# Kernel tuning notes

Measured on AMD Instinct MI355X. Metric: run time of the kernel, lower is better.

## Reference

```python
import jax, jax.numpy as jnp
import numpy as np

B, S, CC, CF, E, H, NH = 16, 1024, 8, 8, 64, 1024, 16
DH = H // NH
VOCAB = 10000
EPS = 1e-5


def layer_norm(x, g, b):
    m = x.mean(-1, keepdims=True)
    v = x.var(-1, keepdims=True)
    return (x - m) / jnp.sqrt(v + EPS) * g + b


def setup_inputs():
    key = jax.random.key(0)
    ks = jax.random.split(key, 30)
    f32 = jnp.float32
    n = lambda k, shp, s=0.02: jax.random.normal(k, shp, f32) * s
    inp = {}
    inp['cate_x'] = jax.random.randint(ks[0], (B, S, CC), 0, VOCAB)
    inp['cont_x'] = jax.random.normal(ks[1], (B, S, CF), f32)
    inp['mask'] = jax.random.randint(ks[2], (B, S), 0, 2)
    # parameters
    inp['emb_table'] = n(ks[3], (VOCAB, E)).at[0].set(0.0)  # padding_idx=0
    inp['cate_W'] = n(ks[4], (CC * E, H)); inp['cate_b'] = jnp.zeros((H,), f32)
    inp['cate_ln_g'] = jnp.ones((H,), f32); inp['cate_ln_b'] = jnp.zeros((H,), f32)
    inp['bn_g'] = jnp.ones((CF,), f32); inp['bn_b'] = jnp.zeros((CF,), f32)
    inp['cont_W'] = n(ks[5], (CF, H)); inp['cont_b'] = jnp.zeros((H,), f32)
    inp['cont_ln_g'] = jnp.ones((H,), f32); inp['cont_ln_b'] = jnp.zeros((H,), f32)
    inp['comb_W'] = n(ks[6], (2 * H, H)); inp['comb_b'] = jnp.zeros((H,), f32)
    inp['comb_ln_g'] = jnp.ones((H,), f32); inp['comb_ln_b'] = jnp.zeros((H,), f32)
    inp['Wq'] = n(ks[7], (H, H)); inp['bq'] = jnp.zeros((H,), f32)
    inp['Wk'] = n(ks[8], (H, H)); inp['bk'] = jnp.zeros((H,), f32)
    inp['Wv'] = n(ks[9], (H, H)); inp['bv'] = jnp.zeros((H,), f32)
    inp['Wo'] = n(ks[10], (H, H)); inp['bo'] = jnp.zeros((H,), f32)
    return inp


def reference(cate_x, cont_x, mask, emb_table, cate_W, cate_b, cate_ln_g, cate_ln_b,
              bn_g, bn_b, cont_W, cont_b, cont_ln_g, cont_ln_b,
              comb_W, comb_b, comb_ln_g, comb_ln_b,
              Wq, bq, Wk, bk, Wv, bv, Wo, bo):
    # categorical path: embed -> flatten cols -> Linear+LN
    cate_emb = emb_table[cate_x].reshape(B, S, CC * E)
    cate_h = layer_norm(cate_emb @ cate_W + cate_b, cate_ln_g, cate_ln_b)
    # continuous path: BatchNorm1d over flattened (B*S, CF) with batch stats
    xf = cont_x.reshape(-1, CF)
    mu = xf.mean(0)
    var = xf.var(0)  # biased, as torch BN normalization
    xn = ((xf - mu) / jnp.sqrt(var + EPS) * bn_g + bn_b).reshape(B, S, CF)
    cont_h = layer_norm(xn @ cont_W + cont_b, cont_ln_g, cont_ln_b)
    # combine: ReLU -> Linear -> LN
    seq = jax.nn.relu(jnp.concatenate([cate_h, cont_h], axis=2))
    x = layer_norm(seq @ comb_W + comb_b, comb_ln_g, comb_ln_b)  # [B,S,H]
    # multi-head attention (dropout is identity in eval)
    Q = (x @ Wq + bq).reshape(B, S, NH, DH)
    K = (x @ Wk + bk).reshape(B, S, NH, DH)
    V = (x @ Wv + bv).reshape(B, S, NH, DH)
    scores = jnp.einsum('bqhd,bkhd->bhqk', Q, K) / np.sqrt(DH).astype(np.float32)
    # faithful to source: mask broadcast over the QUERY axis
    scores = jnp.where(mask[:, None, :, None] == 0, -1e7, scores)
    attn = jax.nn.softmax(scores, axis=-1)
    out = jnp.einsum('bhqk,bkhd->bqhd', attn, V).reshape(B, S, H)
    out = out @ Wo + bo
    return out[:, -1:, -1]  # [B,1]
```

## Files before the change

### kernel.cpp

```cpp
#include <hip/hip_runtime.h>
#include <hip/hip_bf16.h>
#include <math.h>

#define EPS 1e-5f

typedef unsigned short u16;
typedef __attribute__((ext_vector_type(8))) short bf16x8;
typedef __attribute__((ext_vector_type(4))) float f32x4;

__device__ __forceinline__ float b2f(u16 u) {
  union { unsigned int i; float f; } v; v.i = ((unsigned int)u) << 16; return v.f;
}
__device__ __forceinline__ u16 f2b(float f) {
  union { float f; unsigned int i; } v; v.f = f;
  unsigned int r = v.i + 0x7fff + ((v.i >> 16) & 1);
  return (u16)(r >> 16);
}

__device__ __forceinline__ void gload_lds16(const u16* g, u16* l) {
  __builtin_amdgcn_global_load_lds(
      (const __attribute__((address_space(1))) unsigned int*)g,
      (__attribute__((address_space(3))) unsigned int*)l, 16, 0, 0);
}

__global__ __launch_bounds__(256) void prep_k(
    const float* __restrict__ cx, float* __restrict__ part_bn,
    float* __restrict__ outacc, float* __restrict__ Sall,
    const float* __restrict__ emb, u16* __restrict__ embb,
    const float* __restrict__ cate_W, u16* __restrict__ cateWT) {
  __shared__ float shmem[64 * 65];
  const int bid = blockIdx.x, tid = threadIdx.x;

  if (bid == 0) {
    if (tid < 16) outacc[tid] = 0.f;
    for (int i = tid; i < 544; i += 256) Sall[i] = 0.f;
    return;
  }
  if (bid <= 64) {
    int pb = bid - 1;
    int gid = pb * 256 + tid;
    float4 a = ((const float4*)cx)[2 * gid];
    float4 b = ((const float4*)cx)[2 * gid + 1];
    float v[16];
    v[0] = a.x; v[1] = a.y; v[2] = a.z; v[3] = a.w;
    v[4] = b.x; v[5] = b.y; v[6] = b.z; v[7] = b.w;
#pragma unroll
    for (int i = 0; i < 8; ++i) v[8 + i] = v[i] * v[i];
#pragma unroll
    for (int off = 32; off; off >>= 1)
#pragma unroll
      for (int i = 0; i < 16; ++i) v[i] += __shfl_down(v[i], off);
    int l = tid & 63, wv_ = tid >> 6;
    if (l == 0)
#pragma unroll
      for (int i = 0; i < 16; ++i) shmem[wv_ * 16 + i] = v[i];
    __syncthreads();
    if (tid < 16)
      part_bn[pb * 16 + tid] = shmem[tid] + shmem[16 + tid] + shmem[32 + tid] + shmem[48 + tid];
    return;
  }
  if (bid <= 689) {
    int i = (bid - 65) * 256 + tid;
    if (i < 160000) {
      float4 v = ((const float4*)emb)[i];
      ushort4 u; u.x = f2b(v.x); u.y = f2b(v.y); u.z = f2b(v.z); u.w = f2b(v.w);
      ((ushort4*)embb)[i] = u;
    }
    return;
  }
  {
    int local = bid - 690;
    int n0 = (local & 15) * 64, k0 = (local >> 4) * 64;
    int c = tid & 63, r0 = tid >> 6;
#pragma unroll
    for (int i = 0; i < 16; ++i) {
      int r = r0 + i * 4;
      shmem[r * 65 + c] = cate_W[(size_t)(k0 + r) * 1024 + n0 + c];
    }
    __syncthreads();
#pragma unroll
    for (int i = 0; i < 16; ++i) {
      int r = r0 + i * 4;
      cateWT[(size_t)(n0 + r) * 512 + k0 + c] = f2b(shmem[c * 65 + r]);
    }
  }
}

template <int MODE>
__global__ __launch_bounds__(512) void gemm256(
    const u16* __restrict__ A0, const u16* __restrict__ A1,
    const int* __restrict__ idx, const u16* __restrict__ embb,
    const u16* __restrict__ BT, const float* __restrict__ bias,
    u16* __restrict__ C, int K) {
  __shared__ u16 As[2][2][8192];
  __shared__ u16 Bs[2][2][8192];
  __shared__ int sidx[MODE == 1 ? 2048 : 4];
  const int tid = threadIdx.x;
  const int bid = blockIdx.x;
  const int chunk = gridDim.x >> 3;
  const int swz = (bid & 7) * chunk + (bid >> 3);
  const int row0 = (swz >> 2) * 256;
  const int col0 = (swz & 3) * 256;

  const int rr8 = tid >> 3;
  const int p8  = tid & 7;
  const int sl  = p8 ^ (rr8 & 7);

  const int l   = tid & 63;
  const int w   = tid >> 6;
  const int wrh = w >> 2;
  const int wcq = w & 3;
  const int hb  = wcq >> 1;
  const int rbb = (wcq & 1) * 64;
  const int lr  = l & 15;
  const int lk  = l >> 4;

  f32x4 acc[8][4];
#pragma unroll
  for (int m = 0; m < 8; ++m)
#pragma unroll
    for (int n = 0; n < 4; ++n) acc[m][n] = (f32x4){0.f, 0.f, 0.f, 0.f};

  const int nt = K >> 6;
  const int nit = nt >> 1;

  if (MODE == 1) {
    *(int4*)&sidx[tid * 4] = *(const int4*)&idx[row0 * 8 + tid * 4];
    __syncthreads();
  }

  auto stageA = [&](int t, int h) {
    const int k0 = t << 6;
    const int buf = t & 1;
#pragma unroll
    for (int i = 0; i < 2; ++i) {
      const u16* asrc;
      if (MODE == 1) {
        int id = sidx[(h * 128 + i * 64 + rr8) * 8 + (k0 >> 6)];
        asrc = embb + (size_t)id * 64 + sl * 8;
      } else {
        int ar = row0 + h * 128 + i * 64 + rr8;
        const u16* base = (k0 < 1024) ? A0 : A1;
        asrc = base + (size_t)ar * 1024 + (k0 & 1023) + sl * 8;
      }
      gload_lds16(asrc, &As[buf][h][i * 4096 + tid * 8]);
    }
  };
  auto stageB = [&](int t, int h) {
    const int k0 = t << 6;
    const int buf = t & 1;
#pragma unroll
    for (int i = 0; i < 2; ++i) {
      int br = col0 + h * 128 + i * 64 + rr8;
      gload_lds16(BT + (size_t)br * K + k0 + sl * 8,
                  &Bs[buf][h][i * 4096 + tid * 8]);
    }
  };

  bf16x8 bfr[4][2];
  auto loadB = [&](int buf) {
#pragma unroll
    for (int n = 0; n < 4; ++n)
#pragma unroll
      for (int ks = 0; ks < 2; ++ks) {
        int rowb = rbb + n * 16 + lr;
        int ph = (ks * 4 + lk) ^ (lr & 7);
        bfr[n][ks] = *(const bf16x8*)&Bs[buf][hb][rowb * 64 + ph * 8];
      }
  };
  auto loadA = [&](bf16x8 (&af)[2][2], int buf, int q) {
#pragma unroll
    for (int mm = 0; mm < 2; ++mm)
#pragma unroll
      for (int ks = 0; ks < 2; ++ks) {
        int rowa = (q * 2 + mm) * 16 + lr;
        int ph = (ks * 4 + lk) ^ (lr & 7);
        af[mm][ks] = *(const bf16x8*)&As[buf][wrh][rowa * 64 + ph * 8];
      }
  };
  auto mfma_quad = [&](bf16x8 (&af)[2][2], int q) {
    __builtin_amdgcn_s_setprio(1);
#pragma unroll
    for (int ks = 0; ks < 2; ++ks)
#pragma unroll
      for (int mm = 0; mm < 2; ++mm)
#pragma unroll
        for (int n = 0; n < 4; ++n)
          acc[q * 2 + mm][n] = __builtin_amdgcn_mfma_f32_16x16x32_bf16(
              af[mm][ks], bfr[n][ks], acc[q * 2 + mm][n], 0, 0, 0);
    __builtin_amdgcn_s_setprio(0);
  };

  stageA(0, 0); stageA(0, 1);
  stageB(0, 0); stageB(0, 1);
  stageB(1, 0); stageB(1, 1);
  asm volatile("s_waitcnt vmcnt(4)" ::: "memory");
  __builtin_amdgcn_s_barrier();

  for (int it = 0; it < nit; ++it) {
    const int T = it * 2;
    const bool more = (T + 2 < nt);
    bf16x8 af[2][2];

    loadB(0); loadA(af, 0, 0);
    stageA(T + 1, 0);
    __builtin_amdgcn_s_barrier();
    asm volatile("s_waitcnt lgkmcnt(0)" ::: "memory");
    mfma_quad(af, 0);
    __builtin_amdgcn_s_barrier();
    loadA(af, 0, 1);
    stageA(T + 1, 1);
    __builtin_amdgcn_s_barrier();
    asm volatile("s_waitcnt lgkmcnt(0)" ::: "memory");
    mfma_quad(af, 1);
    __builtin_amdgcn_s_barrier();
    loadA(af, 0, 2);
    if (more) stageB(T + 2, 0);
    __builtin_amdgcn_s_barrier();
    asm volatile("s_waitcnt lgkmcnt(0)" ::: "memory");
    mfma_quad(af, 2);
    __builtin_amdgcn_s_barrier();
    loadA(af, 0, 3);
    if (more) stageB(T + 2, 1);
    __builtin_amdgcn_s_barrier();
    asm volatile("s_waitcnt lgkmcnt(0)" ::: "memory");
    mfma_quad(af, 3);
    if (more) asm volatile("s_waitcnt vmcnt(4)" ::: "memory");
    else      asm volatile("s_waitcnt vmcnt(0)" ::: "memory");
    __builtin_amdgcn_s_barrier();

    loadB(1); loadA(af, 1, 0);
    if (more) stageA(T + 2, 0);
    __builtin_amdgcn_s_barrier();
    asm volatile("s_waitcnt lgkmcnt(0)" ::: "memory");
    mfma_quad(af, 0);
    __builtin_amdgcn_s_barrier();
    loadA(af, 1, 1);
    if (more) stageA(T + 2, 1);
    __builtin_amdgcn_s_barrier();
    asm volatile("s_waitcnt lgkmcnt(0)" ::: "memory");
    mfma_quad(af, 1);
    __builtin_amdgcn_s_barrier();
    loadA(af, 1, 2);
    if (more) stageB(T + 3, 0);
    __builtin_amdgcn_s_barrier();
    asm volatile("s_waitcnt lgkmcnt(0)" ::: "memory");
    mfma_quad(af, 2);
    __builtin_amdgcn_s_barrier();
    loadA(af, 1, 3);
    if (more) stageB(T + 3, 1);
    __builtin_amdgcn_s_barrier();
    asm volatile("s_waitcnt lgkmcnt(0)" ::: "memory");
    mfma_quad(af, 3);
    if (it + 1 < nit) {
      asm volatile("s_waitcnt vmcnt(4)" ::: "memory");
      __builtin_amdgcn_s_barrier();
    }
  }

  float bv_[4];
#pragma unroll
  for (int n = 0; n < 4; ++n) bv_[n] = bias[col0 + wcq * 64 + n * 16 + lr];
#pragma unroll
  for (int m = 0; m < 8; ++m) {
#pragma unroll
    for (int n = 0; n < 4; ++n) {
      int cc = col0 + wcq * 64 + n * 16 + lr;
#pragma unroll
      for (int q4 = 0; q4 < 4; ++q4) {
        int rr = row0 + wrh * 128 + m * 16 + lk * 4 + q4;
        C[(size_t)rr * 1024 + cc] = f2b(acc[m][n][q4] + bv_[n]);
      }
    }
  }
}

__global__ __launch_bounds__(256) void stat_k(const u16* __restrict__ buf,
                                              float* __restrict__ stats) {
  int tid = threadIdx.x;
  int lane = tid & 63, wave = tid >> 6;
  size_t row = (size_t)blockIdx.x * 4 + wave;
  const u16* p = buf + row * 1024 + lane * 16;
  uint4 u0 = *(const uint4*)p;
  uint4 u1 = *(const uint4*)(p + 8);
  float s = 0.f, s2 = 0.f;
#pragma unroll
  for (int i = 0; i < 4; ++i) {
    unsigned int w0 = ((unsigned int*)&u0)[i];
    unsigned int w1 = ((unsigned int*)&u1)[i];
    float a0 = b2f((u16)(w0 & 0xffff)), a1 = b2f((u16)(w0 >> 16));
    float a2 = b2f((u16)(w1 & 0xffff)), a3 = b2f((u16)(w1 >> 16));
    s += a0 + a1 + a2 + a3;
    s2 += a0 * a0 + a1 * a1 + a2 * a2 + a3 * a3;
  }
#pragma unroll
  for (int off = 32; off; off >>= 1) { s += __shfl_xor(s, off); s2 += __shfl_xor(s2, off); }
  if (lane == 0) {
    float mean = s * (1.f / 1024.f);
    float var = s2 * (1.f / 1024.f) - mean * mean;
    stats[row * 2] = mean;
    stats[row * 2 + 1] = rsqrtf(var + EPS);
  }
}

__device__ __forceinline__ void ln_body(u16* __restrict__ buf,
                                        const float* __restrict__ g,
                                        const float* __restrict__ b, int relu,
                                        int blk, int tid) {
  int lane = tid & 63, wave = tid >> 6;
  size_t row = (size_t)blk * 4 + wave;
  u16* p = buf + row * 1024 + lane * 16;
  uint4 u0 = *(uint4*)p;
  uint4 u1 = *(uint4*)(p + 8);
  float x[16];
#pragma unroll
  for (int i = 0; i < 4; ++i) {
    unsigned int w0 = ((unsigned int*)&u0)[i];
    unsigned int w1 = ((unsigned int*)&u1)[i];
    x[2 * i]     = b2f((u16)(w0 & 0xffff));
    x[2 * i + 1] = b2f((u16)(w0 >> 16));
    x[8 + 2 * i]     = b2f((u16)(w1 & 0xffff));
    x[8 + 2 * i + 1] = b2f((u16)(w1 >> 16));
  }
  float s = 0.f, s2 = 0.f;
#pragma unroll
  for (int i = 0; i < 16; ++i) { s += x[i]; s2 += x[i] * x[i]; }
#pragma unroll
  for (int off = 32; off; off >>= 1) { s += __shfl_xor(s, off); s2 += __shfl_xor(s2, off); }
  float mean = s * (1.f / 1024.f);
  float var = s2 * (1.f / 1024.f) - mean * mean;
  float rs = rsqrtf(var + EPS);
  float y[16];
#pragma unroll
  for (int q = 0; q < 4; ++q) {
    float4 gv = *(const float4*)(g + lane * 16 + q * 4);
    float4 bv = *(const float4*)(b + lane * 16 + q * 4);
    y[4 * q]     = (x[4 * q]     - mean) * rs * gv.x + bv.x;
    y[4 * q + 1] = (x[4 * q + 1] - mean) * rs * gv.y + bv.y;
    y[4 * q + 2] = (x[4 * q + 2] - mean) * rs * gv.z + bv.z;
    y[4 * q + 3] = (x[4 * q + 3] - mean) * rs * gv.w + bv.w;
  }
  if (relu)
#pragma unroll
    for (int i = 0; i < 16; ++i) y[i] = fmaxf(y[i], 0.f);
  uint4 o0, o1;
#pragma unroll
  for (int i = 0; i < 4; ++i) {
    ((unsigned int*)&o0)[i] = (unsigned int)f2b(y[2 * i]) | ((unsigned int)f2b(y[2 * i + 1]) << 16);
    ((unsigned int*)&o1)[i] = (unsigned int)f2b(y[8 + 2 * i]) | ((unsigned int)f2b(y[8 + 2 * i + 1]) << 16);
  }
  *(uint4*)p = o0;
  *(uint4*)(p + 8) = o1;
}

__device__ __forceinline__ void cont_body(const float* __restrict__ cx,
                                          const float* __restrict__ part_bn,
                                          const float* __restrict__ bn_g,
                                          const float* __restrict__ bn_b,
                                          const float* __restrict__ W,
                                          const float* __restrict__ cb,
                                          const float* __restrict__ g,
                                          const float* __restrict__ bb,
                                          u16* __restrict__ out,
                                          int row0, int tid) {
  __shared__ float sp[4][16];
  __shared__ float tt[16];
  __shared__ float ab[2][8];
  __shared__ float xn[8][8];
  __shared__ float rr1[4][8], rr2[4][8];

  if (tid < 64) {
    int f = tid & 15, qd = tid >> 4;
    float s = 0.f;
    for (int j = qd * 16; j < qd * 16 + 16; ++j) s += part_bn[j * 16 + f];
    sp[qd][f] = s;
  }
  __syncthreads();
  if (tid < 16) tt[tid] = sp[0][tid] + sp[1][tid] + sp[2][tid] + sp[3][tid];
  __syncthreads();
  if (tid < 8) {
    float mu = tt[tid] * (1.f / 16384.f);
    float var = tt[8 + tid] * (1.f / 16384.f) - mu * mu;
    float a = rsqrtf(var + EPS) * bn_g[tid];
    ab[0][tid] = a;
    ab[1][tid] = bn_b[tid] - mu * a;
  }
  __syncthreads();
  if (tid < 64) {
    int r = tid >> 3, f = tid & 7;
    xn[r][f] = ab[0][f] * cx[(row0 + r) * 8 + f] + ab[1][f];
  }
  __syncthreads();

  int c = tid * 4;
  float4 cbv = *(const float4*)(cb + c);
  float acc[8][4];
#pragma unroll
  for (int r = 0; r < 8; ++r) {
    acc[r][0] = cbv.x; acc[r][1] = cbv.y; acc[r][2] = cbv.z; acc[r][3] = cbv.w;
  }
  for (int k = 0; k < 8; ++k) {
    float4 w4 = *(const float4*)(W + k * 1024 + c);
#pragma unroll
    for (int r = 0; r < 8; ++r) {
      float xv = xn[r][k];
      acc[r][0] = fmaf(xv, w4.x, acc[r][0]);
      acc[r][1] = fmaf(xv, w4.y, acc[r][1]);
      acc[r][2] = fmaf(xv, w4.z, acc[r][2]);
      acc[r][3] = fmaf(xv, w4.w, acc[r][3]);
    }
  }
  float s1[8], s2[8];
#pragma unroll
  for (int r = 0; r < 8; ++r) {
    s1[r] = acc[r][0] + acc[r][1] + acc[r][2] + acc[r][3];
    s2[r] = acc[r][0] * acc[r][0] + acc[r][1] * acc[r][1] +
            acc[r][2] * acc[r][2] + acc[r][3] * acc[r][3];
  }
#pragma unroll
  for (int off = 32; off; off >>= 1)
#pragma unroll
    for (int r = 0; r < 8; ++r) {
      s1[r] += __shfl_down(s1[r], off);
      s2[r] += __shfl_down(s2[r], off);
    }
  int lane = tid & 63, wv = tid >> 6;
  if (lane == 0)
#pragma unroll
    for (int r = 0; r < 8; ++r) { rr1[wv][r] = s1[r]; rr2[wv][r] = s2[r]; }
  __syncthreads();
  float4 gv = *(const float4*)(g + c);
  float4 bv = *(const float4*)(bb + c);
#pragma unroll
  for (int r = 0; r < 8; ++r) {
    float ss = rr1[0][r] + rr1[1][r] + rr1[2][r] + rr1[3][r];
    float qq = rr2[0][r] + rr2[1][r] + rr2[2][r] + rr2[3][r];
    float mean = ss * (1.f / 1024.f);
    float var = qq * (1.f / 1024.f) - mean * mean;
    float rs = rsqrtf(var + EPS);
    float y0 = fmaxf((acc[r][0] - mean) * rs * gv.x + bv.x, 0.f);
    float y1 = fmaxf((acc[r][1] - mean) * rs * gv.y + bv.y, 0.f);
    float y2 = fmaxf((acc[r][2] - mean) * rs * gv.z + bv.z, 0.f);
    float y3 = fmaxf((acc[r][3] - mean) * rs * gv.w + bv.w, 0.f);
    ushort4 o; o.x = f2b(y0); o.y = f2b(y1); o.z = f2b(y2); o.w = f2b(y3);
    *(ushort4*)(out + (size_t)(row0 + r) * 1024 + c) = o;
  }
}

__global__ __launch_bounds__(256) void mid_k(
    u16* __restrict__ X1, const float* __restrict__ cate_g,
    const float* __restrict__ cate_bb,
    const float* __restrict__ comb_W, u16* __restrict__ combWT,
    const float* __restrict__ Wv, const float* __restrict__ Wo,
    const float* __restrict__ comb_g, const float* __restrict__ comb_bbv,
    u16* __restrict__ wvob_hi, u16* __restrict__ wvob_lo,
    float* __restrict__ woc, float* __restrict__ Swg, float* __restrict__ Swb,
    const float* __restrict__ cx, const float* __restrict__ part_bn,
    const float* __restrict__ bn_g, const float* __restrict__ bn_b,
    const float* __restrict__ cont_W, const float* __restrict__ cont_b,
    const float* __restrict__ cont_g, const float* __restrict__ cont_bb,
    u16* __restrict__ X2) {
  __shared__ float shmem[64 * 65];
  const int bid = blockIdx.x, tid = threadIdx.x;
  if (bid < 4096) {
    ln_body(X1, cate_g, cate_bb, 1, bid, tid);
    return;
  }
  if (bid < 4608) {
    int local = bid - 4096;
    int n0 = (local & 15) * 64, k0 = (local >> 4) * 64;
    int c = tid & 63, r0 = tid >> 6;
#pragma unroll
    for (int i = 0; i < 16; ++i) {
      int r = r0 + i * 4;
      shmem[r * 65 + c] = comb_W[(size_t)(k0 + r) * 1024 + n0 + c];
    }
    __syncthreads();
#pragma unroll
    for (int i = 0; i < 16; ++i) {
      int r = r0 + i * 4;
      combWT[(size_t)(n0 + r) * 2048 + k0 + c] = f2b(shmem[c * 65 + r]);
    }
    return;
  }
  if (bid < 4672) {
    int local = bid - 4608;
    int h = local >> 2, jc = local & 3;
    if (tid < 64) shmem[tid] = Wo[(size_t)(h * 64 + tid) * 1024 + 1023];
    __syncthreads();
    if (jc == 0 && tid < 64) woc[h * 64 + tid] = shmem[tid];
    int j = jc * 256 + tid;
    const float* vr = Wv + (size_t)j * 1024 + h * 64;
    float s = 0.f;
    for (int d4 = 0; d4 < 64; d4 += 4) {
      float4 w4 = *(const float4*)(vr + d4);
      s = fmaf(w4.x, shmem[d4], s);
      s = fmaf(w4.y, shmem[d4 + 1], s);
      s = fmaf(w4.z, shmem[d4 + 2], s);
      s = fmaf(w4.w, shmem[d4 + 3], s);
    }
    float sg_ = s * comb_g[j];
    u16 hi = f2b(sg_);
    float lo = sg_ - b2f(hi);
    wvob_hi[h * 1024 + j] = hi;
    wvob_lo[h * 1024 + j] = f2b(lo);
    float swgp = sg_;
    float swbp = s * comb_bbv[j];
#pragma unroll
    for (int off = 32; off; off >>= 1) {
      swgp += __shfl_down(swgp, off);
      swbp += __shfl_down(swbp, off);
    }
    int lane = tid & 63, wv = tid >> 6;
    if (lane == 0) { shmem[64 + wv] = swgp; shmem[68 + wv] = swbp; }
    __syncthreads();
    if (tid == 0) {
      atomicAdd(&Swg[h], shmem[64] + shmem[65] + shmem[66] + shmem[67]);
      atomicAdd(&Swb[h], shmem[68] + shmem[69] + shmem[70] + shmem[71]);
    }
    return;
  }
  {
    int row0 = (bid - 4672) * 8;
    cont_body(cx, part_bn, bn_g, bn_b, cont_W, cont_b, cont_g, cont_bb, X2,
              row0, tid);
  }
}

__global__ __launch_bounds__(256) void qproj_k(const u16* __restrict__ x,
                                               const float* __restrict__ stats,
                                               const float* __restrict__ g,
                                               const float* __restrict__ bb,
                                               const float* __restrict__ Wq,
                                               const float* __restrict__ bq,
                                               float* __restrict__ q) {
  __shared__ u16 xs[16][1024];
  __shared__ float part[16][16][16];
  __shared__ float sm[16], sr[16];
  int tid = threadIdx.x;
  if (tid < 16) {
    size_t row = (size_t)tid * 1024 + 1023;
    sm[tid] = stats[row * 2];
    sr[tid] = stats[row * 2 + 1];
  }
  __syncthreads();
  for (int i = tid; i < 4096; i += 256) {
    int b = i >> 8, off = (i & 255) * 4;
    ushort4 u =
        *(const ushort4*)(x + ((size_t)(b * 1024 + 1023)) * 1024 + off);
    float4 gv = *(const float4*)(g + off);
    float4 bv = *(const float4*)(bb + off);
    float m = sm[b], r = sr[b];
    ushort4 o;
    o.x = f2b((b2f(u.x) - m) * r * gv.x + bv.x);
    o.y = f2b((b2f(u.y) - m) * r * gv.y + bv.y);
    o.z = f2b((b2f(u.z) - m) * r * gv.z + bv.z);
    o.w = f2b((b2f(u.w) - m) * r * gv.w + bv.w);
    *(ushort4*)&xs[b][off] = o;
  }
  __syncthreads();
  int c = tid & 15;
  int col = blockIdx.x * 16 + c;
  int kq = tid >> 4;
  float acc[16];
#pragma unroll
  for (int b = 0; b < 16; ++b) acc[b] = 0.f;
  for (int k = kq * 64; k < kq * 64 + 64; ++k) {
    float wv = Wq[(size_t)k * 1024 + col];
#pragma unroll
    for (int b = 0; b < 16; ++b) acc[b] = fmaf(b2f(xs[b][k]), wv, acc[b]);
  }
#pragma unroll
  for (int b = 0; b < 16; ++b) part[kq][b][c] = acc[b];
  __syncthreads();
  {
    int b = tid >> 4, cc = tid & 15;
    float s = 0.f;
#pragma unroll
    for (int j = 0; j < 16; ++j) s += part[j][b][cc];
    q[b * 1024 + blockIdx.x * 16 + cc] = s + bq[blockIdx.x * 16 + cc];
  }
}

__global__ __launch_bounds__(256) void kq_k(const float* __restrict__ Wk,
                                            const float* __restrict__ bk,
                                            const float* __restrict__ q,
                                            const float* __restrict__ g,
                                            const float* __restrict__ bb,
                                            u16* __restrict__ qtb,
                                            float* __restrict__ bkq,
                                            float* __restrict__ Sg,
                                            float* __restrict__ Sb) {
  int h = blockIdx.x >> 2, jc = blockIdx.x & 3;
  int tid = threadIdx.x;
  __shared__ float Qs[16][64];
  __shared__ float rg[4][16], rb[4][16];
  for (int i = tid; i < 1024; i += 256) {
    int b = i >> 6, d = i & 63;
    Qs[b][d] = q[b * 1024 + h * 64 + d];
  }
  __syncthreads();
  int j = jc * 256 + tid;
  float acc[16];
#pragma unroll
  for (int b = 0; b < 16; ++b) acc[b] = 0.f;
  const float* wr = Wk + (size_t)j * 1024 + h * 64;
  for (int d4 = 0; d4 < 64; d4 += 4) {
    float4 w4 = *(const float4*)(wr + d4);
#pragma unroll
    for (int b = 0; b < 16; ++b) {
      acc[b] = fmaf(w4.x, Qs[b][d4], acc[b]);
      acc[b] = fmaf(w4.y, Qs[b][d4 + 1], acc[b]);
      acc[b] = fmaf(w4.z, Qs[b][d4 + 2], acc[b]);
      acc[b] = fmaf(w4.w, Qs[b][d4 + 3], acc[b]);
    }
  }
  float gj = g[j], bbj = bb[j];
  float sgp[16], sbp[16];
#pragma unroll
  for (int b = 0; b < 16; ++b) {
    u16 qg = f2b(acc[b] * gj);
    qtb[((size_t)b * 16 + h) * 1024 + j] = qg;
    sgp[b] = b2f(qg);
    sbp[b] = acc[b] * bbj;
  }
#pragma unroll
  for (int off = 32; off; off >>= 1)
#pragma unroll
    for (int b = 0; b < 16; ++b) {
      sgp[b] += __shfl_down(sgp[b], off);
      sbp[b] += __shfl_down(sbp[b], off);
    }
  int lane = tid & 63, wv = tid >> 6;
  if (lane == 0)
#pragma unroll
    for (int b = 0; b < 16; ++b) { rg[wv][b] = sgp[b]; rb[wv][b] = sbp[b]; }
  __syncthreads();
  if (tid < 16) {
    int b = tid;
    atomicAdd(&Sg[b * 16 + h], rg[0][b] + rg[1][b] + rg[2][b] + rg[3][b]);
    atomicAdd(&Sb[b * 16 + h], rb[0][b] + rb[1][b] + rb[2][b] + rb[3][b]);
  }
  if (jc == 0 && tid < 16) {
    int b = tid;
    float s = 0.f;
    for (int d = 0; d < 64; ++d) s = fmaf(bk[h * 64 + d], Qs[b][d], s);
    bkq[b * 16 + h] = s;
  }
}

__global__ __launch_bounds__(256) void score_k(
    const u16* __restrict__ x, const u16* __restrict__ qtb,
    const float* __restrict__ bkq, const int* __restrict__ mask,
    const u16* __restrict__ whi, const u16* __restrict__ wlo,
    const float* __restrict__ stats,
    const float* __restrict__ Sg, const float* __restrict__ Sb,
    const float* __restrict__ Swg, const float* __restrict__ Swb,
    float* __restrict__ sc, float* __restrict__ y) {
  int b = blockIdx.x >> 4, kc = blockIdx.x & 15;
  int tid = threadIdx.x;
  int l = tid & 63, w = tid >> 6;
  int keybase = kc * 64 + w * 16;
  int lr = l & 15, ls = l >> 4;
  int masked = (mask[b * 1024 + 1023] == 0);

  f32x4 acc = (f32x4){0.f, 0.f, 0.f, 0.f};
  f32x4 acy = (f32x4){0.f, 0.f, 0.f, 0.f};
  const u16* xb = x + (size_t)b * 1024 * 1024;
  const u16* qb = qtb + (size_t)b * 16 * 1024;
  for (int k0 = 0; k0 < 1024; k0 += 32) {
    bf16x8 bfr = *(const bf16x8*)&qb[(size_t)lr * 1024 + k0 + ls * 8];
    bf16x8 bh  = *(const bf16x8*)&whi[(size_t)lr * 1024 + k0 + ls * 8];
    bf16x8 bl  = *(const bf16x8*)&wlo[(size_t)lr * 1024 + k0 + ls * 8];
    bf16x8 afr = *(const bf16x8*)&xb[(size_t)(keybase + lr) * 1024 + k0 + ls * 8];
    acc = __builtin_amdgcn_mfma_f32_16x16x32_bf16(afr, bfr, acc, 0, 0, 0);
    acy = __builtin_amdgcn_mfma_f32_16x16x32_bf16(afr, bh, acy, 0, 0, 0);
    acy = __builtin_amdgcn_mfma_f32_16x16x32_bf16(afr, bl, acy, 0, 0, 0);
  }
  int h = lr;
  float bq_  = bkq[b * 16 + h];
  float Sgv  = Sg[b * 16 + h];
  float Sbv  = Sb[b * 16 + h];
  float Swgv = Swg[h];
  float Swbv = Swb[h];
#pragma unroll
  for (int q = 0; q < 4; ++q) {
    int key = keybase + ls * 4 + q;
    size_t row = (size_t)b * 1024 + key;
    float mean = stats[row * 2];
    float rs   = stats[row * 2 + 1];
    float sraw = rs * acc[q] - rs * mean * Sgv + Sbv + bq_;
    float v = masked ? 0.f : sraw * 0.125f;
    sc[((size_t)b * 16 + h) * 1024 + key] = v;
    y[((size_t)b * 16 + h) * 1024 + key] =
        rs * acy[q] - rs * mean * Swgv + Swbv;
  }
}

__global__ __launch_bounds__(256) void fin_k(const float* __restrict__ sc,
                                             const float* __restrict__ y,
                                             float* __restrict__ outacc) {
  int bh = blockIdx.x, tid = threadIdx.x;
  float4 v = ((const float4*)(sc + (size_t)bh * 1024))[tid];
  float m = fmaxf(fmaxf(v.x, v.y), fmaxf(v.z, v.w));
#pragma unroll
  for (int off = 32; off; off >>= 1) m = fmaxf(m, __shfl_down(m, off));
  __shared__ float rm[4], rs_[4], rd_[4];
  int lane = tid & 63, wv = tid >> 6;
  if (lane == 0) rm[wv] = m;
  __syncthreads();
  m = fmaxf(fmaxf(rm[0], rm[1]), fmaxf(rm[2], rm[3]));
  float e0 = expf(v.x - m), e1 = expf(v.y - m), e2 = expf(v.z - m), e3 = expf(v.w - m);
  float4 yv = ((const float4*)(y + (size_t)bh * 1024))[tid];
  float s = e0 + e1 + e2 + e3;
  float d = e0 * yv.x + e1 * yv.y + e2 * yv.z + e3 * yv.w;
#pragma unroll
  for (int off = 32; off; off >>= 1) {
    s += __shfl_down(s, off);
    d += __shfl_down(d, off);
  }
  if (lane == 0) { rs_[wv] = s; rd_[wv] = d; }
  __syncthreads();
  if (tid == 0) {
    float Z = rs_[0] + rs_[1] + rs_[2] + rs_[3];
    float D = rd_[0] + rd_[1] + rd_[2] + rd_[3];
    atomicAdd(&outacc[bh >> 4], D / Z);
  }
}

__global__ __launch_bounds__(256) void bfinal_k(const float* __restrict__ outacc,
                                                const float* __restrict__ bv,
                                                const float* __restrict__ woc,
                                                const float* __restrict__ bo,
                                                float* __restrict__ out) {
  int tid = threadIdx.x;
  float s = 0.f;
  for (int i = tid; i < 1024; i += 256) s = fmaf(bv[i], woc[i], s);
#pragma unroll
  for (int off = 32; off; off >>= 1) s += __shfl_down(s, off);
  __shared__ float r[4];
  int lane = tid & 63, wv = tid >> 6;
  if (lane == 0) r[wv] = s;
  __syncthreads();
  float bc = r[0] + r[1] + r[2] + r[3] + bo[1023];
  if (tid < 16) out[tid] = outacc[tid] + bc;
}

extern "C" void kernel_launch(void* const* d_in, const int* in_sizes, int n_in,
                              void* d_out, int out_size, void* d_ws, size_t ws_size,
                              hipStream_t stream) {
  const int*   cate_x  = (const int*)d_in[0];
  const float* cont_x  = (const float*)d_in[1];
  const int*   mask    = (const int*)d_in[2];
  const float* emb     = (const float*)d_in[3];
  const float* cate_W  = (const float*)d_in[4];
  const float* cate_b  = (const float*)d_in[5];
  const float* cate_g  = (const float*)d_in[6];
  const float* cate_bb = (const float*)d_in[7];
  const float* bn_g    = (const float*)d_in[8];
  const float* bn_b    = (const float*)d_in[9];
  const float* cont_W  = (const float*)d_in[10];
  const float* cont_b  = (const float*)d_in[11];
  const float* cont_g  = (const float*)d_in[12];
  const float* cont_bb = (const float*)d_in[13];
  const float* Wq = (const float*)d_in[18]; const float* bq = (const float*)d_in[19];
  const float* Wk = (const float*)d_in[20]; const float* bk = (const float*)d_in[21];
  const float* Wv = (const float*)d_in[22]; const float* bv = (const float*)d_in[23];
  const float* Wo = (const float*)d_in[24]; const float* bo = (const float*)d_in[25];
  const float* comb_W  = (const float*)d_in[14];
  const float* comb_b  = (const float*)d_in[15];
  const float* comb_g  = (const float*)d_in[16];
  const float* comb_bb = (const float*)d_in[17];
  float* out = (float*)d_out;

  char* w = (char*)d_ws;
  float* stats0  = (float*)w;
  float* outacc  = stats0 + 16;
  float* part_bn = (float*)(w + 256);
  float* qbuf    = (float*)(w + 8192);
  u16* embb      = (u16*)(w + 131328);
  u16* cateWT    = (u16*)(w + 1411328);
  u16* combWT    = (u16*)(w + 2459904);
  float* sc      = (float*)(w + 6654208);
  u16*   qtb     = (u16*)(w + 7702784);
  float* bkq     = (float*)(w + 8292608);
  float* ybuf    = (float*)(w + 8388608);
  u16* wvob_hi   = (u16*)(w + 9437184);
  u16* wvob_lo   = (u16*)(w + 9469952);
  float* woc     = (float*)(w + 9502720);
  float* lstats  = (float*)(w + 10031104);
  float* Sall    = (float*)(w + 10162176);
  float* Sg      = Sall;
  float* Sb      = Sall + 256;
  float* Swg     = Sall + 512;
  float* Swb     = Sall + 528;
  u16* X1        = (u16*)(w + 10848512);
  u16* X2        = X1 + (size_t)16777216;
  u16* xb        = X2 + (size_t)16777216;

  prep_k<<<818, 256, 0, stream>>>(cont_x, part_bn, outacc, Sall, emb, embb,
                                  cate_W, cateWT);

  gemm256<1><<<256, 512, 0, stream>>>(nullptr, nullptr, cate_x, embb, cateWT,
                                      cate_b, X1, 512);
  mid_k<<<6720, 256, 0, stream>>>(X1, cate_g, cate_bb, comb_W, combWT, Wv, Wo,
                                  comb_g, comb_bb, wvob_hi, wvob_lo, woc, Swg,
                                  Swb, cont_x, part_bn, bn_g, bn_b, cont_W,
                                  cont_b, cont_g, cont_bb, X2);
  gemm256<2><<<256, 512, 0, stream>>>(X1, X2, nullptr, nullptr, combWT,
                                      comb_b, xb, 2048);
  stat_k<<<4096, 256, 0, stream>>>(xb, lstats);

  qproj_k<<<64, 256, 0, stream>>>(xb, lstats, comb_g, comb_bb, Wq, bq, qbuf);
  kq_k<<<64, 256, 0, stream>>>(Wk, bk, qbuf, comb_g, comb_bb, qtb, bkq, Sg, Sb);
  score_k<<<256, 256, 0, stream>>>(xb, qtb, bkq, mask, wvob_hi, wvob_lo,
                                   lstats, Sg, Sb, Swg, Swb, sc, ybuf);
  fin_k<<<256, 256, 0, stream>>>(sc, ybuf, outacc);
  bfinal_k<<<1, 256, 0, stream>>>(outacc, bv, woc, bo, out);
}
```

Measured before the change: 191.7 us.

## Fuse LayerNorm row statistics into score and qproj kernels, drop stat_k

Removes the separate stat_k pass, which read the entire bf16 combined activation buffer only to compute per-row mean and rstd. score_k now gets row sums from an extra MFMA against a vector of bf16 ones, and sums of squares from the diagonal of an A·Aᵀ MFMA, pulled out with a lane shuffle. qproj_k computes stats for its 16 last-position rows itself from LDS. This saves a full pass over 32 MB and one launch, at the cost of two extra MFMAs per k-step in score_k.

After: 189.5 us. Within noise of the previous version (-1.1%).

```diff
diff --git a/kernel.cpp b/kernel.cpp
--- a/kernel.cpp
+++ b/kernel.cpp
@@ -272,34 +272,6 @@
         C[(size_t)rr * 1024 + cc] = f2b(acc[m][n][q4] + bv_[n]);
       }
     }
-  }
-}
-
-__global__ __launch_bounds__(256) void stat_k(const u16* __restrict__ buf,
-                                              float* __restrict__ stats) {
-  int tid = threadIdx.x;
-  int lane = tid & 63, wave = tid >> 6;
-  size_t row = (size_t)blockIdx.x * 4 + wave;
-  const u16* p = buf + row * 1024 + lane * 16;
-  uint4 u0 = *(const uint4*)p;
-  uint4 u1 = *(const uint4*)(p + 8);
-  float s = 0.f, s2 = 0.f;
-#pragma unroll
-  for (int i = 0; i < 4; ++i) {
-    unsigned int w0 = ((unsigned int*)&u0)[i];
-    unsigned int w1 = ((unsigned int*)&u1)[i];
-    float a0 = b2f((u16)(w0 & 0xffff)), a1 = b2f((u16)(w0 >> 16));
-    float a2 = b2f((u16)(w1 & 0xffff)), a3 = b2f((u16)(w1 >> 16));
-    s += a0 + a1 + a2 + a3;
-    s2 += a0 * a0 + a1 * a1 + a2 * a2 + a3 * a3;
-  }
-#pragma unroll
-  for (int off = 32; off; off >>= 1) { s += __shfl_xor(s, off); s2 += __shfl_xor(s2, off); }
-  if (lane == 0) {
-    float mean = s * (1.f / 1024.f);
-    float var = s2 * (1.f / 1024.f) - mean * mean;
-    stats[row * 2] = mean;
-    stats[row * 2 + 1] = rsqrtf(var + EPS);
   }
 }
 
@@ -528,7 +500,6 @@
 }
 
 __global__ __launch_bounds__(256) void qproj_k(const u16* __restrict__ x,
-                                               const float* __restrict__ stats,
                                                const float* __restrict__ g,
                                                const float* __restrict__ bb,
                                                const float* __restrict__ Wq,
@@ -536,18 +507,40 @@
                                                float* __restrict__ q) {
   __shared__ u16 xs[16][1024];
   __shared__ float part[16][16][16];
+  __shared__ float ps1[16][16], ps2[16][16];
   __shared__ float sm[16], sr[16];
   int tid = threadIdx.x;
-  if (tid < 16) {
-    size_t row = (size_t)tid * 1024 + 1023;
-    sm[tid] = stats[row * 2];
-    sr[tid] = stats[row * 2 + 1];
-  }
-  __syncthreads();
   for (int i = tid; i < 4096; i += 256) {
     int b = i >> 8, off = (i & 255) * 4;
-    ushort4 u =
+    *(ushort4*)&xs[b][off] =
         *(const ushort4*)(x + ((size_t)(b * 1024 + 1023)) * 1024 + off);
+  }
+  __syncthreads();
+  {
+    int b = tid >> 4, seg = tid & 15;
+    float s = 0.f, s2 = 0.f;
+    for (int k = seg * 64; k < seg * 64 + 64; ++k) {
+      float v = b2f(xs[b][k]);
+      s += v;
+      s2 = fmaf(v, v, s2);
+    }
+    ps1[b][seg] = s;
+    ps2[b][seg] = s2;
+  }
+  __syncthreads();
+  if (tid < 16) {
+    float s = 0.f, s2 = 0.f;
+#pragma unroll
+    for (int j = 0; j < 16; ++j) { s += ps1[tid][j]; s2 += ps2[tid][j]; }
+    float mean = s * (1.f / 1024.f);
+    float var = s2 * (1.f / 1024.f) - mean * mean;
+    sm[tid] = mean;
+    sr[tid] = rsqrtf(var + EPS);
+  }
+  __syncthreads();
+  for (int i = tid; i < 4096; i += 256) {
+    int b = i >> 8, off = (i & 255) * 4;
+    ushort4 u = *(ushort4*)&xs[b][off];
     float4 gv = *(const float4*)(g + off);
     float4 bv = *(const float4*)(bb + off);
     float m = sm[b], r = sr[b];
@@ -653,7 +646,6 @@
     const u16* __restrict__ x, const u16* __restrict__ qtb,
     const float* __restrict__ bkq, const int* __restrict__ mask,
     const u16* __restrict__ whi, const u16* __restrict__ wlo,
-    const float* __restrict__ stats,
     const float* __restrict__ Sg, const float* __restrict__ Sb,
     const float* __restrict__ Swg, const float* __restrict__ Swb,
     float* __restrict__ sc, float* __restrict__ y) {
@@ -664,8 +656,14 @@
   int lr = l & 15, ls = l >> 4;
   int masked = (mask[b * 1024 + 1023] == 0);
 
+  bf16x8 ones;
+#pragma unroll
+  for (int j = 0; j < 8; ++j) ones[j] = (short)0x3F80;
+
   f32x4 acc = (f32x4){0.f, 0.f, 0.f, 0.f};
   f32x4 acy = (f32x4){0.f, 0.f, 0.f, 0.f};
+  f32x4 as1 = (f32x4){0.f, 0.f, 0.f, 0.f};
+  f32x4 as2 = (f32x4){0.f, 0.f, 0.f, 0.f};
   const u16* xb = x + (size_t)b * 1024 * 1024;
   const u16* qb = qtb + (size_t)b * 16 * 1024;
   for (int k0 = 0; k0 < 1024; k0 += 32) {
@@ -676,6 +674,8 @@
     acc = __builtin_amdgcn_mfma_f32_16x16x32_bf16(afr, bfr, acc, 0, 0, 0);
     acy = __builtin_amdgcn_mfma_f32_16x16x32_bf16(afr, bh, acy, 0, 0, 0);
     acy = __builtin_amdgcn_mfma_f32_16x16x32_bf16(afr, bl, acy, 0, 0, 0);
+    as1 = __builtin_amdgcn_mfma_f32_16x16x32_bf16(afr, ones, as1, 0, 0, 0);
+    as2 = __builtin_amdgcn_mfma_f32_16x16x32_bf16(afr, afr, as2, 0, 0, 0);
   }
   int h = lr;
   float bq_  = bkq[b * 16 + h];
@@ -686,9 +686,11 @@
 #pragma unroll
   for (int q = 0; q < 4; ++q) {
     int key = keybase + ls * 4 + q;
-    size_t row = (size_t)b * 1024 + key;
-    float mean = stats[row * 2];
-    float rs   = stats[row * 2 + 1];
+    float s1 = as1[q];
+    float s2 = __shfl(as2[q], ls * 4 + q + 16 * ls);
+    float mean = s1 * (1.f / 1024.f);
+    float var  = s2 * (1.f / 1024.f) - mean * mean;
+    float rs   = rsqrtf(var + EPS);
     float sraw = rs * acc[q] - rs * mean * Sgv + Sbv + bq_;
     float v = masked ? 0.f : sraw * 0.125f;
     sc[((size_t)b * 16 + h) * 1024 + key] = v;
@@ -788,7 +790,6 @@
   u16* wvob_hi   = (u16*)(w + 9437184);
   u16* wvob_lo   = (u16*)(w + 9469952);
   float* woc     = (float*)(w + 9502720);
-  float* lstats  = (float*)(w + 10031104);
   float* Sall    = (float*)(w + 10162176);
   float* Sg      = Sall;
   float* Sb      = Sall + 256;
@@ -809,12 +810,11 @@
                                   cont_b, cont_g, cont_bb, X2);
   gemm256<2><<<256, 512, 0, stream>>>(X1, X2, nullptr, nullptr, combWT,
                                       comb_b, xb, 2048);
-  stat_k<<<4096, 256, 0, stream>>>(xb, lstats);
-
-  qproj_k<<<64, 256, 0, stream>>>(xb, lstats, comb_g, comb_bb, Wq, bq, qbuf);
+
+  qproj_k<<<64, 256, 0, stream>>>(xb, comb_g, comb_bb, Wq, bq, qbuf);
   kq_k<<<64, 256, 0, stream>>>(Wk, bk, qbuf, comb_g, comb_bb, qtb, bkq, Sg, Sb);
   score_k<<<256, 256, 0, stream>>>(xb, qtb, bkq, mask, wvob_hi, wvob_lo,
-                                   lstats, Sg, Sb, Swg, Swb, sc, ybuf);
+                                   Sg, Sb, Swg, Swb, sc, ybuf);
   fin_k<<<256, 256, 0, stream>>>(sc, ybuf, outacc);
   bfinal_k<<<1, 256, 0, stream>>>(outacc, bv, woc, bo, out);
 }
```
